# Kernel tuning notes

Hardware: AMD Instinct MI355X
Metric: run time of the kernel (lower is better)

The kernel has to match this reference:

```python
import jax, jax.numpy as jnp
import numpy as np

B, K, T, C = 4, 8, 2048, 64

def setup_inputs() -> dict:
    key = jax.random.key(0)
    ks = jax.random.split(key, 7)
    return {
        "x": jax.random.normal(ks[0], (B, K, T, C), dtype=jnp.float32),
        "Wq": jax.random.normal(ks[1], (C, C), dtype=jnp.float32) / np.sqrt(C),
        "bq": jax.random.normal(ks[2], (C,), dtype=jnp.float32) * 0.01,
        "Wk": jax.random.normal(ks[3], (C, C), dtype=jnp.float32) / np.sqrt(C),
        "bk": jax.random.normal(ks[4], (C,), dtype=jnp.float32) * 0.01,
        "Wv": jax.random.normal(ks[5], (C, C), dtype=jnp.float32) / np.sqrt(C),
        "bv": jax.random.normal(ks[6], (C,), dtype=jnp.float32) * 0.01,
    }

def reference(x, Wq, bq, Wk, bk, Wv, bv):
    c_dim = x.shape[-1]
    # torch nn.Linear: y = x @ W.T + b
    q = jnp.einsum('bktc,dc->bktd', x, Wq) + bq
    k = jnp.einsum('bktc,dc->bktd', x, Wk) + bk
    v = jnp.einsum('bktc,dc->bktd', x, Wv) + bv
    scores = jnp.einsum('bkic,bkjc->bkij', q, k) / jnp.sqrt(jnp.float32(c_dim))
    attn = jax.nn.softmax(scores, axis=-1)
    out = jnp.einsum('bkij,bkjc->bkic', attn, v)
    return out
```

## Files before the change

### kernel.cpp

```cpp
#include <hip/hip_runtime.h>


#define T_DIM 2048
#define NHEAD 32
#define HSTRIDE (T_DIM * 64)
#define QSCALE 0.18033688011112042f
#define SOFF  8.0f

#define SWZ(row, grp) ((row) * 64 + ((((grp) ^ ((row) & 7)) & 7) * 8))

typedef _Float16 h8 __attribute__((ext_vector_type(8)));
typedef _Float16 h4 __attribute__((ext_vector_type(4)));
typedef __fp16   g2 __attribute__((ext_vector_type(2)));
typedef float    f4 __attribute__((ext_vector_type(4)));

union H4U { h4 v; g2 p[2]; };
union H8U { h8 v; h4 h[2]; };

#if defined(__has_builtin)
#if __has_builtin(__builtin_amdgcn_exp2f)
#define EXP2(x) __builtin_amdgcn_exp2f(x)
#endif
#endif
#ifndef EXP2
__device__ inline float exp2_raw(float x) {
    float r;
    asm("v_exp_f32 %0, %1" : "=v"(r) : "v"(x));
    return r;
}
#define EXP2(x) exp2_raw(x)
#endif

__device__ inline h4 cvt4(f4 x) {
    H4U u;
    u.p[0] = __builtin_amdgcn_cvt_pkrtz(x[0], x[1]);
    u.p[1] = __builtin_amdgcn_cvt_pkrtz(x[2], x[3]);
    return u.v;
}

__device__ inline h8 cvt8(f4 a, f4 b) {
    H8U r;
    r.h[0] = cvt4(a);
    r.h[1] = cvt4(b);
    return r.v;
}

__global__ __launch_bounds__(256) void qkv_proj_kernel(
    const float* __restrict__ x,
    const float* __restrict__ Wq, const float* __restrict__ bq,
    const float* __restrict__ Wk, const float* __restrict__ bk,
    const float* __restrict__ Wv, const float* __restrict__ bv,
    _Float16* __restrict__ qh, _Float16* __restrict__ khT,
    _Float16* __restrict__ vtT)
{
    __shared__ _Float16 ws[3][64 * 64];
    __shared__ _Float16 ot[64 * 64];
    __shared__ float bsh[3][64];

    const int tid  = threadIdx.x;
    const int row0 = blockIdx.x * 64;
    const int head = blockIdx.x >> 5;
    const int t0   = (blockIdx.x & 31) * 64;

    #pragma unroll
    for (int m = 0; m < 3; ++m) {
        const float* Wm = (m == 0) ? Wq : ((m == 1) ? Wk : Wv);
        const float* bm = (m == 0) ? bq : ((m == 1) ? bk : bv);
        #pragma unroll
        for (int pass = 0; pass < 4; ++pass) {
            const int idx = pass * 1024 + tid * 4;
            const int d = idx >> 6, c = idx & 63;
            f4 wv = *(const f4*)(Wm + idx);
            *(h4*)&ws[m][SWZ(d, c >> 3) + (c & 7)] = cvt4(wv);
        }
        if (tid < 64) bsh[m][tid] = bm[tid];
    }

    const int w    = tid >> 6;
    const int lane = tid & 63;
    const int l15  = lane & 15;
    const int qd   = lane >> 4;

    h8 af[2];
    {
        const float* xp = x + (size_t)(row0 + w * 16 + l15) * 64 + qd * 8;
        #pragma unroll
        for (int ch = 0; ch < 2; ++ch) {
            f4 a0 = *(const f4*)(xp + ch * 32);
            f4 a1 = *(const f4*)(xp + ch * 32 + 4);
            af[ch] = cvt8(a0, a1);
        }
    }
    __syncthreads();

    #pragma unroll
    for (int m = 0; m < 3; ++m) {
        h8 bf[4][2];
        #pragma unroll
        for (int ns = 0; ns < 4; ++ns)
            #pragma unroll
            for (int ch = 0; ch < 2; ++ch)
                bf[ns][ch] = *(const h8*)&ws[m][SWZ(ns * 16 + l15, ch * 4 + qd)];

        f4 acc[4];
        #pragma unroll
        for (int ns = 0; ns < 4; ++ns)
            acc[ns] = (f4){0.f, 0.f, 0.f, 0.f};
        #pragma unroll
        for (int ch = 0; ch < 2; ++ch)
            #pragma unroll
            for (int ns = 0; ns < 4; ++ns)
                acc[ns] = __builtin_amdgcn_mfma_f32_16x16x32_f16(
                    af[ch], bf[ns][ch], acc[ns], 0, 0, 0);

        __syncthreads();
        if (m < 2) {
            #pragma unroll
            for (int ns = 0; ns < 4; ++ns) {
                const int d = ns * 16 + l15;
                const float bias = bsh[m][d];
                #pragma unroll
                for (int r = 0; r < 4; ++r) {
                    const int t = w * 16 + qd * 4 + r;
                    float v = acc[ns][r] + bias;
                    if (m == 0) v *= QSCALE;
                    ot[SWZ(t, d >> 3) + (d & 7)] = (_Float16)v;
                }
            }
            __syncthreads();
            if (m == 0) {
                #pragma unroll
                for (int pass = 0; pass < 2; ++pass) {
                    const int t  = pass * 32 + (tid >> 3);
                    const int c0 = (tid & 7) * 8;
                    *(h8*)&qh[(size_t)(row0 + t) * 64 + c0] =
                        *(const h8*)&ot[SWZ(t, tid & 7)];
                }
            } else {
                #pragma unroll
                for (int pass = 0; pass < 2; ++pass) {
                    const int f    = pass * 2048 + tid * 8;
                    const int Jl   = f >> 10;
                    const int rest = f & 1023;
                    const int ch_  = rest >> 9;
                    const int qd_  = (rest >> 7) & 3;
                    const int l15_ = (rest >> 3) & 15;
                    h8 val = *(const h8*)&ot[SWZ(Jl * 16 + l15_, ch_ * 4 + qd_)];
                    *(h8*)&khT[(size_t)head * HSTRIDE + ((t0 >> 4) + Jl) * 1024 + rest] = val;
                }
            }
        } else {
            #pragma unroll
            for (int ns = 0; ns < 4; ++ns) {
                const int d = ns * 16 + l15;
                const float bias = bsh[2][d];
                const int tl = w * 16 + qd * 4;
                f4 pvf;
                #pragma unroll
                for (int r = 0; r < 4; ++r)
                    pvf[r] = acc[ns][r] + bias;
                *(h4*)&ot[SWZ(d, tl >> 3) + (tl & 7)] = cvt4(pvf);
            }
            __syncthreads();
            #pragma unroll
            for (int pass = 0; pass < 2; ++pass) {
                const int f   = pass * 2048 + tid * 8;
                const int qd3 = f >> 10;
                const int rem = f & 1023;
                const int c   = rem >> 4;
                const int g   = (rem & 15) >> 3;
                const int ta  = (2 * g) * 16 + qd3 * 4;
                const int tb  = ta + 16;
                H8U val;
                val.h[0] = *(const h4*)&ot[SWZ(c, ta >> 3) + (ta & 7)];
                val.h[1] = *(const h4*)&ot[SWZ(c, tb >> 3) + (tb & 7)];
                *(h8*)&vtT[(size_t)head * HSTRIDE + (t0 >> 6) * 4096 + f] = val.v;
            }
        }
    }
}

__global__ __launch_bounds__(512, 2) void attn_kernel(
    const _Float16* __restrict__ qh, const _Float16* __restrict__ khT,
    const _Float16* __restrict__ vtT, float* __restrict__ out)
{
    __shared__ float mrg[2][64][41];
    const int tid  = threadIdx.x;
    const int w    = tid >> 6;
    const int lane = tid & 63;
    const int l15  = lane & 15;
    const int qd   = lane >> 4;
    const int qgrp = w & 1;
    const int kph  = w >> 1;

    const int bid  = blockIdx.x;
    const int xcd  = bid & 7;
    const int slot = bid >> 3;
    const int head = xcd * 4 + (slot >> 5);
    const int q0   = (slot & 31) * 64 + qgrp * 32;

    h8 qf[2][2];
    #pragma unroll
    for (int is = 0; is < 2; ++is) {
        const _Float16* qp = qh + (size_t)(head * T_DIM + q0 + is * 16 + l15) * 64 + qd * 8;
        qf[is][0] = *(const h8*)qp;
        qf[is][1] = *(const h8*)(qp + 32);
    }

    const h4 vones = {(_Float16)1.0f, (_Float16)1.0f, (_Float16)1.0f, (_Float16)1.0f};
    f4 lacc[2] = {(f4){0.f,0.f,0.f,0.f}, (f4){0.f,0.f,0.f,0.f}};
    f4 oacc[2][4];
    #pragma unroll
    for (int is = 0; is < 2; ++is)
        #pragma unroll
        for (int cs = 0; cs < 4; ++cs)
            oacc[is][cs] = (f4){0.f, 0.f, 0.f, 0.f};

    const _Float16* kA = khT + (size_t)head * HSTRIDE + kph * 32768;
    const _Float16* kB = kA + 2048;
    const _Float16* vA = vtT + (size_t)head * HSTRIDE + kph * 32768;
    const int ko = lane * 8;
    const int vo = qd * 1024 + l15 * 16;

    h8 kf[4][2];
    #pragma unroll
    for (int jt = 0; jt < 4; ++jt)
        #pragma unroll
        for (int ch = 0; ch < 2; ++ch)
            kf[jt][ch] = *(const h8*)(((jt < 2) ? kA : kB) + (jt & 1) * 1024 + ch * 512 + ko);

    for (int kt = 0; kt < 8; ++kt) {
        H8U vf8[4][2];
        #pragma unroll
        for (int cs = 0; cs < 4; ++cs) {
            vf8[cs][0].v = *(const h8*)(vA + cs * 256 + vo);
            vf8[cs][1].v = *(const h8*)(vA + cs * 256 + vo + 8);
        }

        f4 st[4][2];
        #pragma unroll
        for (int jt = 0; jt < 4; ++jt)
            #pragma unroll
            for (int is = 0; is < 2; ++is)
                st[jt][is] = (f4){-SOFF, -SOFF, -SOFF, -SOFF};
        #pragma unroll
        for (int ch = 0; ch < 2; ++ch)
            #pragma unroll
            for (int jt = 0; jt < 4; ++jt)
                #pragma unroll
                for (int is = 0; is < 2; ++is)
                    st[jt][is] = __builtin_amdgcn_mfma_f32_16x16x32_f16(
                        kf[jt][ch], qf[is][ch], st[jt][is], 0, 0, 0);

        kA += 4096; kB += 4096;
        if (kt < 7) {
            #pragma unroll
            for (int jt = 0; jt < 4; ++jt)
                #pragma unroll
                for (int ch = 0; ch < 2; ++ch)
                    kf[jt][ch] = *(const h8*)(((jt < 2) ? kA : kB) + (jt & 1) * 1024 + ch * 512 + ko);
        }

        h4 pf[4][2];
        #pragma unroll
        for (int is = 0; is < 2; ++is)
            #pragma unroll
            for (int jt = 0; jt < 4; ++jt) {
                f4 p;
                p[0] = EXP2(st[jt][is][0]);
                p[1] = EXP2(st[jt][is][1]);
                p[2] = EXP2(st[jt][is][2]);
                p[3] = EXP2(st[jt][is][3]);
                pf[jt][is] = cvt4(p);
            }

        #pragma unroll
        for (int jt = 0; jt < 4; ++jt) {
            #pragma unroll
            for (int cs = 0; cs < 4; ++cs)
                #pragma unroll
                for (int is = 0; is < 2; ++is)
                    oacc[is][cs] = __builtin_amdgcn_mfma_f32_16x16x16f16(
                        pf[jt][is], vf8[cs][jt >> 1].h[jt & 1], oacc[is][cs], 0, 0, 0);
            #pragma unroll
            for (int is = 0; is < 2; ++is)
                lacc[is] = __builtin_amdgcn_mfma_f32_16x16x16f16(
                    pf[jt][is], vones, lacc[is], 0, 0, 0);
        }
        vA += 4096;
    }

    #pragma unroll
    for (int src = 3; src >= 1; --src) {
        if (kph == src) {
            #pragma unroll
            for (int is = 0; is < 2; ++is) {
                #pragma unroll
                for (int cs = 0; cs < 4; ++cs)
                    #pragma unroll
                    for (int r = 0; r < 4; ++r)
                        mrg[qgrp][lane][(is * 4 + cs) * 4 + r] = oacc[is][cs][r];
                #pragma unroll
                for (int r = 0; r < 4; ++r)
                    mrg[qgrp][lane][32 + is * 4 + r] = lacc[is][r];
            }
        }
        __syncthreads();
        if (kph == 0) {
            #pragma unroll
            for (int is = 0; is < 2; ++is) {
                #pragma unroll
                for (int cs = 0; cs < 4; ++cs)
                    #pragma unroll
                    for (int r = 0; r < 4; ++r)
                        oacc[is][cs][r] += mrg[qgrp][lane][(is * 4 + cs) * 4 + r];
                #pragma unroll
                for (int r = 0; r < 4; ++r)
                    lacc[is][r] += mrg[qgrp][lane][32 + is * 4 + r];
            }
        }
        if (src > 1) __syncthreads();
    }

    if (kph == 0) {
        #pragma unroll
        for (int is = 0; is < 2; ++is) {
            float linv[4];
            #pragma unroll
            for (int r = 0; r < 4; ++r)
                linv[r] = 1.f / lacc[is][r];
            #pragma unroll
            for (int cs = 0; cs < 4; ++cs) {
                const int c = cs * 16 + l15;
                #pragma unroll
                for (int r = 0; r < 4; ++r) {
                    const int t = q0 + is * 16 + qd * 4 + r;
                    out[(size_t)(head * T_DIM + t) * 64 + c] = oacc[is][cs][r] * linv[r];
                }
            }
        }
    }
}

extern "C" void kernel_launch(void* const* d_in, const int* in_sizes, int n_in,
                              void* d_out, int out_size, void* d_ws, size_t ws_size,
                              hipStream_t stream)
{
    (void)in_sizes; (void)n_in; (void)out_size; (void)ws_size;
    const float* x  = (const float*)d_in[0];
    const float* Wq = (const float*)d_in[1];
    const float* bq = (const float*)d_in[2];
    const float* Wk = (const float*)d_in[3];
    const float* bk = (const float*)d_in[4];
    const float* Wv = (const float*)d_in[5];
    const float* bv = (const float*)d_in[6];
    float* out = (float*)d_out;

    _Float16* qh  = (_Float16*)d_ws;
    _Float16* khT = qh + (size_t)NHEAD * HSTRIDE;
    _Float16* vtT = khT + (size_t)NHEAD * HSTRIDE;

    hipLaunchKernelGGL(qkv_proj_kernel, dim3(1024), dim3(256), 0, stream,
                       x, Wq, bq, Wk, bk, Wv, bv, qh, khT, vtT);
    hipLaunchKernelGGL(attn_kernel, dim3(1024), dim3(512), 0, stream,
                       qh, khT, vtT, out);
}
```

Baseline: 132.9 us.

## Stage K/V tiles in shared memory and share them across four query groups

The attention kernel now processes 128 queries per block (4 query groups × 2 key phases) instead of 64 queries across 4 key phases. Each iteration cooperatively loads K and V tiles into LDS, with register prefetch of the next tile, and all waves read their fragments from LDS. This cuts redundant global/L2 traffic for K and V and halves the grid. The cross-phase merge is reduced to a single exchange between two phases. The cost is two barriers per iteration, LDS reads on the MFMA critical path, and fewer blocks for latency hiding.

```diff
diff --git a/kernel.cpp b/kernel.cpp
--- a/kernel.cpp
+++ b/kernel.cpp
@@ -184,20 +184,24 @@
     const _Float16* __restrict__ qh, const _Float16* __restrict__ khT,
     const _Float16* __restrict__ vtT, float* __restrict__ out)
 {
-    __shared__ float mrg[2][64][41];
+    __shared__ long long smem_ll[5120];
+    _Float16* tiles = (_Float16*)smem_ll;
+    float*    mrgO  = (float*)smem_ll;
+    float*    mrgL  = (float*)smem_ll + 8192;
+
     const int tid  = threadIdx.x;
     const int w    = tid >> 6;
     const int lane = tid & 63;
     const int l15  = lane & 15;
     const int qd   = lane >> 4;
-    const int qgrp = w & 1;
-    const int kph  = w >> 1;
+    const int qgrp = w >> 1;
+    const int kph  = w & 1;
 
     const int bid  = blockIdx.x;
     const int xcd  = bid & 7;
     const int slot = bid >> 3;
-    const int head = xcd * 4 + (slot >> 5);
-    const int q0   = (slot & 31) * 64 + qgrp * 32;
+    const int head = xcd * 4 + (slot >> 4);
+    const int q0   = (slot & 15) * 128 + qgrp * 32;
 
     h8 qf[2][2];
     #pragma unroll
@@ -216,25 +220,37 @@
         for (int cs = 0; cs < 4; ++cs)
             oacc[is][cs] = (f4){0.f, 0.f, 0.f, 0.f};
 
-    const _Float16* kA = khT + (size_t)head * HSTRIDE + kph * 32768;
-    const _Float16* kB = kA + 2048;
-    const _Float16* vA = vtT + (size_t)head * HSTRIDE + kph * 32768;
+    const _Float16* kT = khT + (size_t)head * HSTRIDE;
+    const _Float16* vT = vtT + (size_t)head * HSTRIDE;
+    const int G  = tid >> 6;
+    const int ld = tid & 63;
+    const int vsrcoff = (ld >> 4) * 1024 + ((G >> 1) * 16 + (ld & 15)) * 16 + (G & 1) * 8;
+    const _Float16* s0 = kT + tid * 8;
+    const _Float16* s1 = kT + 16 * 4096 + tid * 8;
+    const _Float16* s2 = vT + vsrcoff;
+    const _Float16* s3 = vT + 16 * 4096 + vsrcoff;
+    _Float16* d0 = tiles + tid * 8;
+    _Float16* d1 = tiles + 4096 + tid * 8;
+    _Float16* d2 = tiles + 8192 + G * 512 + ld * 8;
+    _Float16* d3 = d2 + 4096;
+
+    const _Float16* kb = tiles + kph * 4096;
+    const _Float16* vb = tiles + 8192 + kph * 4096;
     const int ko = lane * 8;
-    const int vo = qd * 1024 + l15 * 16;
-
-    h8 kf[4][2];
-    #pragma unroll
-    for (int jt = 0; jt < 4; ++jt)
-        #pragma unroll
-        for (int ch = 0; ch < 2; ++ch)
-            kf[jt][ch] = *(const h8*)(((jt < 2) ? kA : kB) + (jt & 1) * 1024 + ch * 512 + ko);
-
-    for (int kt = 0; kt < 8; ++kt) {
-        H8U vf8[4][2];
-        #pragma unroll
-        for (int cs = 0; cs < 4; ++cs) {
-            vf8[cs][0].v = *(const h8*)(vA + cs * 256 + vo);
-            vf8[cs][1].v = *(const h8*)(vA + cs * 256 + vo + 8);
+
+    h8 sr0 = *(const h8*)s0, sr1 = *(const h8*)s1;
+    h8 sr2 = *(const h8*)s2, sr3 = *(const h8*)s3;
+    s0 += 4096; s1 += 4096; s2 += 4096; s3 += 4096;
+
+    for (int it = 0; it < 16; ++it) {
+        __syncthreads();
+        *(h8*)d0 = sr0; *(h8*)d1 = sr1;
+        *(h8*)d2 = sr2; *(h8*)d3 = sr3;
+        __syncthreads();
+        if (it < 15) {
+            sr0 = *(const h8*)s0; sr1 = *(const h8*)s1;
+            sr2 = *(const h8*)s2; sr3 = *(const h8*)s3;
+            s0 += 4096; s1 += 4096; s2 += 4096; s3 += 4096;
         }
 
         f4 st[4][2];
@@ -246,20 +262,13 @@
         #pragma unroll
         for (int ch = 0; ch < 2; ++ch)
             #pragma unroll
-            for (int jt = 0; jt < 4; ++jt)
+            for (int jt = 0; jt < 4; ++jt) {
+                h8 kf = *(const h8*)(kb + jt * 1024 + ch * 512 + ko);
                 #pragma unroll
                 for (int is = 0; is < 2; ++is)
                     st[jt][is] = __builtin_amdgcn_mfma_f32_16x16x32_f16(
-                        kf[jt][ch], qf[is][ch], st[jt][is], 0, 0, 0);
-
-        kA += 4096; kB += 4096;
-        if (kt < 7) {
-            #pragma unroll
-            for (int jt = 0; jt < 4; ++jt)
-                #pragma unroll
-                for (int ch = 0; ch < 2; ++ch)
-                    kf[jt][ch] = *(const h8*)(((jt < 2) ? kA : kB) + (jt & 1) * 1024 + ch * 512 + ko);
-        }
+                        kf, qf[is][ch], st[jt][is], 0, 0, 0);
+            }
 
         h4 pf[4][2];
         #pragma unroll
@@ -275,67 +284,64 @@
             }
 
         #pragma unroll
-        for (int jt = 0; jt < 4; ++jt) {
-            #pragma unroll
-            for (int cs = 0; cs < 4; ++cs)
-                #pragma unroll
-                for (int is = 0; is < 2; ++is)
-                    oacc[is][cs] = __builtin_amdgcn_mfma_f32_16x16x16f16(
-                        pf[jt][is], vf8[cs][jt >> 1].h[jt & 1], oacc[is][cs], 0, 0, 0);
+        for (int cs = 0; cs < 4; ++cs) {
+            H8U v0, v1;
+            v0.v = *(const h8*)(vb + (cs * 2 + 0) * 512 + ko);
+            v1.v = *(const h8*)(vb + (cs * 2 + 1) * 512 + ko);
+            #pragma unroll
+            for (int is = 0; is < 2; ++is) {
+                oacc[is][cs] = __builtin_amdgcn_mfma_f32_16x16x16f16(
+                    pf[0][is], v0.h[0], oacc[is][cs], 0, 0, 0);
+                oacc[is][cs] = __builtin_amdgcn_mfma_f32_16x16x16f16(
+                    pf[1][is], v0.h[1], oacc[is][cs], 0, 0, 0);
+                oacc[is][cs] = __builtin_amdgcn_mfma_f32_16x16x16f16(
+                    pf[2][is], v1.h[0], oacc[is][cs], 0, 0, 0);
+                oacc[is][cs] = __builtin_amdgcn_mfma_f32_16x16x16f16(
+                    pf[3][is], v1.h[1], oacc[is][cs], 0, 0, 0);
+            }
+        }
+        #pragma unroll
+        for (int jt = 0; jt < 4; ++jt)
             #pragma unroll
             for (int is = 0; is < 2; ++is)
                 lacc[is] = __builtin_amdgcn_mfma_f32_16x16x16f16(
                     pf[jt][is], vones, lacc[is], 0, 0, 0);
-        }
-        vA += 4096;
-    }
-
-    #pragma unroll
-    for (int src = 3; src >= 1; --src) {
-        if (kph == src) {
-            #pragma unroll
-            for (int is = 0; is < 2; ++is) {
-                #pragma unroll
-                for (int cs = 0; cs < 4; ++cs)
-                    #pragma unroll
-                    for (int r = 0; r < 4; ++r)
-                        mrg[qgrp][lane][(is * 4 + cs) * 4 + r] = oacc[is][cs][r];
+    }
+
+    __syncthreads();
+    if (kph == 1) {
+        float* po = mrgO + (qgrp * 64 + lane) * 32;
+        float* pl = mrgL + (qgrp * 64 + lane) * 8;
+        #pragma unroll
+        for (int is = 0; is < 2; ++is) {
+            #pragma unroll
+            for (int cs = 0; cs < 4; ++cs)
                 #pragma unroll
                 for (int r = 0; r < 4; ++r)
-                    mrg[qgrp][lane][32 + is * 4 + r] = lacc[is][r];
-            }
-        }
-        __syncthreads();
-        if (kph == 0) {
-            #pragma unroll
-            for (int is = 0; is < 2; ++is) {
-                #pragma unroll
-                for (int cs = 0; cs < 4; ++cs)
-                    #pragma unroll
-                    for (int r = 0; r < 4; ++r)
-                        oacc[is][cs][r] += mrg[qgrp][lane][(is * 4 + cs) * 4 + r];
-                #pragma unroll
-                for (int r = 0; r < 4; ++r)
-                    lacc[is][r] += mrg[qgrp][lane][32 + is * 4 + r];
-            }
-        }
-        if (src > 1) __syncthreads();
-    }
-
+                    po[(is * 4 + cs) * 4 + r] = oacc[is][cs][r];
+            #pragma unroll
+            for (int r = 0; r < 4; ++r)
+                pl[is * 4 + r] = lacc[is][r];
+        }
+    }
+    __syncthreads();
     if (kph == 0) {
+        const float* po = mrgO + (qgrp * 64 + lane) * 32;
+        const float* pl = mrgL + (qgrp * 64 + lane) * 8;
         #pragma unroll
         for (int is = 0; is < 2; ++is) {
             float linv[4];
             #pragma unroll
             for (int r = 0; r < 4; ++r)
-                linv[r] = 1.f / lacc[is][r];
+                linv[r] = 1.f / (lacc[is][r] + pl[is * 4 + r]);
             #pragma unroll
             for (int cs = 0; cs < 4; ++cs) {
                 const int c = cs * 16 + l15;
                 #pragma unroll
                 for (int r = 0; r < 4; ++r) {
                     const int t = q0 + is * 16 + qd * 4 + r;
-                    out[(size_t)(head * T_DIM + t) * 64 + c] = oacc[is][cs][r] * linv[r];
+                    float o = oacc[is][cs][r] + po[(is * 4 + cs) * 4 + r];
+                    out[(size_t)(head * T_DIM + t) * 64 + c] = o * linv[r];
                 }
             }
         }
@@ -362,6 +368,6 @@
 
     hipLaunchKernelGGL(qkv_proj_kernel, dim3(1024), dim3(256), 0, stream,
                        x, Wq, bq, Wk, bk, Wv, bv, qh, khT, vtT);
-    hipLaunchKernelGGL(attn_kernel, dim3(1024), dim3(512), 0, stream,
+    hipLaunchKernelGGL(attn_kernel, dim3(512), dim3(512), 0, stream,
                        qh, khT, vtT, out);
 }
```

Result: faster. 129.5 us (-2.5%).
